# Kernel optimization log

Measured on AMD Instinct MI355X. Metric: run time of the kernel, lower is better.

The kernel has to match this reference:

```python
import jax, jax.numpy as jnp
import numpy as np

ATOMS_PER_RES = 24  # hard-coded in .view(B, N_l, -1, 24)
NEG_SLOPE = 0.01    # nn.LeakyReLU default


def setup_inputs() -> dict:
    key = jax.random.key(0)
    ks = jax.random.split(key, 10)
    B, N_l, N_p, H, G = 16, 64, 512, 128, 10
    pos_l = jax.random.normal(ks[0], (B, N_l, 3), jnp.float32) * 5.0
    pos_p = jax.random.normal(ks[1], (B, N_p, ATOMS_PER_RES, 3), jnp.float32) * 5.0
    Interact = jax.random.normal(ks[2], (B, N_l, N_p, H), jnp.float32)
    Interact_mask = jax.random.randint(ks[3], (B, N_l, N_p), 0, 2) > 0
    W_pi = jax.random.normal(ks[4], (H, G), jnp.float32) * 0.05
    b_pi = jnp.zeros((G,), jnp.float32)
    W_sigma = jax.random.normal(ks[5], (H, G), jnp.float32) * 0.05
    b_sigma = jnp.zeros((G,), jnp.float32)
    W_mu = jax.random.normal(ks[6], (H, G), jnp.float32) * 0.05
    b_mu = jnp.zeros((G,), jnp.float32)
    return {
        "pos_l": pos_l, "pos_p": pos_p, "Interact": Interact,
        "Interact_mask": Interact_mask,
        "W_pi": W_pi, "b_pi": b_pi,
        "W_sigma": W_sigma, "b_sigma": b_sigma,
        "W_mu": W_mu, "b_mu": b_mu,
    }


def _min_dist(pos_l, pos_p):
    # pos_l: [B, N_l, 3]; pos_p: [B, N_p, 24, 3]
    B, N_l, _ = pos_l.shape
    Y = pos_p.reshape(B, -1, 3)  # [B, N_p*24, 3]
    d2 = (jnp.sum(pos_l * pos_l, axis=-1)[..., None]
          + jnp.sum(Y * Y, axis=-1)[:, None, :]
          - 2.0 * jnp.einsum('bic,bjc->bij', pos_l, Y))  # [B, N_l, N_p*24]
    dist = jnp.nan_to_num(jnp.sqrt(d2), nan=10000.0)
    # min over the 24 atoms of each residue -> [B, N_l, N_p]
    return dist.reshape(B, N_l, -1, ATOMS_PER_RES).min(axis=-1)


def reference(pos_l, pos_p, Interact, Interact_mask,
              W_pi, b_pi, W_sigma, b_sigma, W_mu, b_mu):
    leaky = lambda x: jax.nn.leaky_relu(x, NEG_SLOPE)
    dist = _min_dist(pos_l, pos_p)                       # [B, N_l, N_p]
    # original gathers dist[Interact_mask]; keep static shape, zero-fill masked-out
    dist_masked = jnp.where(Interact_mask, dist, 0.0)
    pi = jax.nn.softmax(Interact @ W_pi + b_pi, axis=-1)          # [B,N_l,N_p,G]
    sigma = jnp.clip(leaky(Interact @ W_sigma + b_sigma) + 1.1, 1e-6, None)
    mu = leaky(Interact @ W_mu + b_mu) + 1.0
    return pi, sigma, mu, dist_masked, Interact_mask
```

## Files before the change

kernel.cpp:

```cpp
#include <hip/hip_runtime.h>
#include <cmath>

#define NB 16
#define NL 64
#define NP 512
#define NH 128
#define NG 10
#define ROWS (NB * NL * NP)

#define OFF_PI    ((size_t)0)
#define OFF_SIGMA ((size_t)5242880)
#define OFF_MU    ((size_t)10485760)
#define OFF_DIST  ((size_t)15728640)
#define OFF_MASK  ((size_t)16252928)

__global__ __launch_bounds__(256, 4) void k_fused(
    const float* __restrict__ pos_l,
    const float* __restrict__ pos_p,
    const int*   __restrict__ mask,
    const float* __restrict__ X,
    const float* __restrict__ Wpi, const float* __restrict__ bpi,
    const float* __restrict__ Wsg, const float* __restrict__ bsg,
    const float* __restrict__ Wmu, const float* __restrict__ bmu,
    float* __restrict__ out_pi,
    float* __restrict__ out_sg,
    float* __restrict__ out_mu,
    float* __restrict__ dist_out,
    float* __restrict__ mask_out)
{
    __shared__ float xs[256 * 33];

    const int tid = threadIdx.x;
    const int idx = blockIdx.x * 256 + tid;

    {
        int p  = idx & (NP - 1);
        int bl = idx >> 9;
        int b  = bl >> 6;

        const float* xl = pos_l + bl * 3;
        float x0 = xl[0], x1 = xl[1], x2 = xl[2];
        float qs = x0 * x0 + x1 * x1 + x2 * x2;

        const float4* yp = (const float4*)(pos_p + ((size_t)(b * NP + p)) * 72);

        float m2 = 1e30f;
        #pragma unroll
        for (int q = 0; q < 6; ++q) {
            float4 v0 = yp[q * 3 + 0];
            float4 v1 = yp[q * 3 + 1];
            float4 v2 = yp[q * 3 + 2];
            float c[12] = {v0.x, v0.y, v0.z, v0.w,
                           v1.x, v1.y, v1.z, v1.w,
                           v2.x, v2.y, v2.z, v2.w};
            #pragma unroll
            for (int a = 0; a < 4; ++a) {
                float yx = c[a * 3 + 0], yy = c[a * 3 + 1], yz = c[a * 3 + 2];
                float d2 = qs + (yx * yx + yy * yy + yz * yz)
                              - 2.0f * (x0 * yx + x1 * yy + x2 * yz);
                d2 = (d2 >= 0.0f) ? d2 : 1e8f;
                m2 = fminf(m2, d2);
            }
        }
        float m = sqrtf(m2);

        int mk = mask[idx];
        dist_out[idx] = mk ? m : 0.0f;
        mask_out[idx] = mk ? 1.0f : 0.0f;
    }

    float accp[NG], accs[NG], accm[NG];
    #pragma unroll
    for (int g = 0; g < NG; ++g) {
        accp[g] = bpi[g];
        accs[g] = bsg[g];
        accm[g] = bmu[g];
    }

    const size_t row0 = (size_t)blockIdx.x * 256;

    for (int kc = 0; kc < 4; ++kc) {
        __syncthreads();
        #pragma unroll
        for (int j = 0; j < 8; ++j) {
            int s  = j * 256 + tid;
            int r  = s >> 3;
            int k4 = s & 7;
            float4 v = *(const float4*)(X + (row0 + r) * NH + kc * 32 + k4 * 4);
            float* d = &xs[r * 33 + k4 * 4];
            d[0] = v.x; d[1] = v.y; d[2] = v.z; d[3] = v.w;
        }
        __syncthreads();

        const float* xr = &xs[tid * 33];
        #pragma unroll 4
        for (int k = 0; k < 32; ++k) {
            float h = xr[k];
            int kk = kc * 32 + k;
            const float* wp = Wpi + kk * NG;
            const float* ws = Wsg + kk * NG;
            const float* wm = Wmu + kk * NG;
            #pragma unroll
            for (int g = 0; g < NG; ++g) {
                accp[g] = fmaf(h, wp[g], accp[g]);
                accs[g] = fmaf(h, ws[g], accs[g]);
                accm[g] = fmaf(h, wm[g], accm[g]);
            }
        }
    }

    size_t ro = (size_t)idx * NG;

    float mx = accp[0];
    #pragma unroll
    for (int g = 1; g < NG; ++g) mx = fmaxf(mx, accp[g]);
    float e[NG], ssum = 0.0f;
    #pragma unroll
    for (int g = 0; g < NG; ++g) { e[g] = __expf(accp[g] - mx); ssum += e[g]; }
    float inv = 1.0f / ssum;
    #pragma unroll
    for (int g = 0; g < NG; ++g) out_pi[ro + g] = e[g] * inv;

    #pragma unroll
    for (int g = 0; g < NG; ++g) {
        float x = accs[g];
        float v = (x >= 0.0f ? x : 0.01f * x) + 1.1f;
        out_sg[ro + g] = fmaxf(v, 1e-6f);
    }

    #pragma unroll
    for (int g = 0; g < NG; ++g) {
        float x = accm[g];
        out_mu[ro + g] = (x >= 0.0f ? x : 0.01f * x) + 1.0f;
    }
}

extern "C" void kernel_launch(void* const* d_in, const int* in_sizes, int n_in,
                              void* d_out, int out_size, void* d_ws, size_t ws_size,
                              hipStream_t stream) {
    const float* pos_l    = (const float*)d_in[0];
    const float* pos_p    = (const float*)d_in[1];
    const float* Interact = (const float*)d_in[2];
    const int*   mask     = (const int*)  d_in[3];
    const float* Wpi      = (const float*)d_in[4];
    const float* bpi      = (const float*)d_in[5];
    const float* Wsg      = (const float*)d_in[6];
    const float* bsg      = (const float*)d_in[7];
    const float* Wmu      = (const float*)d_in[8];
    const float* bmu      = (const float*)d_in[9];

    float* out      = (float*)d_out;
    float* out_pi   = out + OFF_PI;
    float* out_sg   = out + OFF_SIGMA;
    float* out_mu   = out + OFF_MU;
    float* out_dist = out + OFF_DIST;
    float* out_mask = out + OFF_MASK;

    hipLaunchKernelGGL(k_fused, dim3(ROWS / 256), dim3(256), 0, stream,
                       pos_l, pos_p, mask, Interact,
                       Wpi, bpi, Wsg, bsg, Wmu, bmu,
                       out_pi, out_sg, out_mu, out_dist, out_mask);
}
```

Baseline: 427.4 us.

## Prefetch next Interact chunk into registers, vectorize LDS and output stores

The global loads for the first chunk of Interact are now issued at kernel start, before the distance computation, and the next chunk's loads are issued before the FMA loop, so global memory latency overlaps with compute. The LDS row pad changes from 33 to 36 floats, which allows float4 writes into shared memory and float4 reads back out. The outputs are written as float2 stores. The cost is 32 extra registers held for the prefetch buffer, which may reduce occupancy under the 256x4 launch bounds.

```diff
diff --git a/kernel.cpp b/kernel.cpp
--- a/kernel.cpp
+++ b/kernel.cpp
@@ -14,6 +14,8 @@
 #define OFF_DIST  ((size_t)15728640)
 #define OFF_MASK  ((size_t)16252928)
 
+#define XPAD 36
+
 __global__ __launch_bounds__(256, 4) void k_fused(
     const float* __restrict__ pos_l,
     const float* __restrict__ pos_p,
@@ -28,10 +30,24 @@
     float* __restrict__ dist_out,
     float* __restrict__ mask_out)
 {
-    __shared__ float xs[256 * 33];
+    __shared__ __align__(16) float xs[256 * XPAD];
 
     const int tid = threadIdx.x;
     const int idx = blockIdx.x * 256 + tid;
+    const size_t row0 = (size_t)blockIdx.x * 256;
+
+    int sr[8], sk[8];
+    #pragma unroll
+    for (int j = 0; j < 8; ++j) {
+        int s = j * 256 + tid;
+        sr[j] = s >> 3;
+        sk[j] = s & 7;
+    }
+
+    float4 pf[8];
+    #pragma unroll
+    for (int j = 0; j < 8; ++j)
+        pf[j] = *(const float4*)(X + (row0 + sr[j]) * NH + sk[j] * 4);
 
     {
         int p  = idx & (NP - 1);
@@ -77,39 +93,43 @@
         accm[g] = bmu[g];
     }
 
-    const size_t row0 = (size_t)blockIdx.x * 256;
-
     for (int kc = 0; kc < 4; ++kc) {
         __syncthreads();
         #pragma unroll
-        for (int j = 0; j < 8; ++j) {
-            int s  = j * 256 + tid;
-            int r  = s >> 3;
-            int k4 = s & 7;
-            float4 v = *(const float4*)(X + (row0 + r) * NH + kc * 32 + k4 * 4);
-            float* d = &xs[r * 33 + k4 * 4];
-            d[0] = v.x; d[1] = v.y; d[2] = v.z; d[3] = v.w;
-        }
+        for (int j = 0; j < 8; ++j)
+            *(float4*)&xs[sr[j] * XPAD + sk[j] * 4] = pf[j];
         __syncthreads();
 
-        const float* xr = &xs[tid * 33];
-        #pragma unroll 4
-        for (int k = 0; k < 32; ++k) {
-            float h = xr[k];
-            int kk = kc * 32 + k;
-            const float* wp = Wpi + kk * NG;
-            const float* ws = Wsg + kk * NG;
-            const float* wm = Wmu + kk * NG;
+        if (kc < 3) {
             #pragma unroll
-            for (int g = 0; g < NG; ++g) {
-                accp[g] = fmaf(h, wp[g], accp[g]);
-                accs[g] = fmaf(h, ws[g], accs[g]);
-                accm[g] = fmaf(h, wm[g], accm[g]);
+            for (int j = 0; j < 8; ++j)
+                pf[j] = *(const float4*)(X + (row0 + sr[j]) * NH
+                                           + (kc + 1) * 32 + sk[j] * 4);
+        }
+
+        const float4* xr4 = (const float4*)&xs[tid * XPAD];
+        #pragma unroll
+        for (int k4 = 0; k4 < 8; ++k4) {
+            float4 h4 = xr4[k4];
+            float hk[4] = {h4.x, h4.y, h4.z, h4.w};
+            #pragma unroll
+            for (int kk = 0; kk < 4; ++kk) {
+                int kg = kc * 32 + k4 * 4 + kk;
+                const float* wp = Wpi + kg * NG;
+                const float* ws = Wsg + kg * NG;
+                const float* wm = Wmu + kg * NG;
+                float h = hk[kk];
+                #pragma unroll
+                for (int g = 0; g < NG; ++g) {
+                    accp[g] = fmaf(h, wp[g], accp[g]);
+                    accs[g] = fmaf(h, ws[g], accs[g]);
+                    accm[g] = fmaf(h, wm[g], accm[g]);
+                }
             }
         }
     }
 
-    size_t ro = (size_t)idx * NG;
+    const size_t ro = (size_t)idx * NG;
 
     float mx = accp[0];
     #pragma unroll
@@ -119,20 +139,29 @@
     for (int g = 0; g < NG; ++g) { e[g] = __expf(accp[g] - mx); ssum += e[g]; }
     float inv = 1.0f / ssum;
     #pragma unroll
-    for (int g = 0; g < NG; ++g) out_pi[ro + g] = e[g] * inv;
+    for (int g = 0; g < 5; ++g)
+        *(float2*)&out_pi[ro + 2 * g] = make_float2(e[2 * g] * inv,
+                                                    e[2 * g + 1] * inv);
 
+    float sg[NG];
     #pragma unroll
     for (int g = 0; g < NG; ++g) {
         float x = accs[g];
-        float v = (x >= 0.0f ? x : 0.01f * x) + 1.1f;
-        out_sg[ro + g] = fmaxf(v, 1e-6f);
+        sg[g] = fmaxf((x >= 0.0f ? x : 0.01f * x) + 1.1f, 1e-6f);
     }
+    #pragma unroll
+    for (int g = 0; g < 5; ++g)
+        *(float2*)&out_sg[ro + 2 * g] = make_float2(sg[2 * g], sg[2 * g + 1]);
 
+    float mu[NG];
     #pragma unroll
     for (int g = 0; g < NG; ++g) {
         float x = accm[g];
-        out_mu[ro + g] = (x >= 0.0f ? x : 0.01f * x) + 1.0f;
+        mu[g] = (x >= 0.0f ? x : 0.01f * x) + 1.0f;
     }
+    #pragma unroll
+    for (int g = 0; g < 5; ++g)
+        *(float2*)&out_mu[ro + 2 * g] = make_float2(mu[2 * g], mu[2 * g + 1]);
 }
 
 extern "C" void kernel_launch(void* const* d_in, const int* in_sizes, int n_in,
```

Result: slower. 467.7 us (+9.4%).
